# Performance work log

Measured on AMD Instinct MI355X. Metric: run time of the kernel, lower is better.

Reference implementation:

```python
import jax, jax.numpy as jnp
import numpy as np

D_MODEL = 512
NHEAD = 8
HEAD_DIM = D_MODEL // NHEAD
NS = 1  # num_special_tokens


def setup_inputs() -> dict:
    key = jax.random.key(0)
    ks = jax.random.split(key, 12)
    B, N = 8, 1024
    x = jax.random.normal(ks[0], (B, N, D_MODEL), dtype=jnp.float32)
    coords = jax.random.normal(ks[1], (B, N, 3), dtype=jnp.float32) * 5.0
    key_padding_mask = jnp.zeros((B, N), dtype=bool)
    s = 1.0 / np.sqrt(D_MODEL)
    qkv_w = jax.random.normal(ks[2], (3 * D_MODEL, D_MODEL), dtype=jnp.float32) * s
    out_w = jax.random.normal(ks[3], (D_MODEL, D_MODEL), dtype=jnp.float32) * s
    out_b = jnp.zeros((D_MODEL,), dtype=jnp.float32)
    bias_alpha = jnp.ones((1,), dtype=jnp.float32) * 0.5  # nonzero so bias path matters
    w1 = jax.random.normal(ks[4], (NHEAD * 4, 4), dtype=jnp.float32) * 0.5
    b1 = jnp.zeros((NHEAD * 4,), dtype=jnp.float32)
    w2 = jax.random.normal(ks[5], (NHEAD, NHEAD * 4), dtype=jnp.float32) * 0.2
    b2 = jnp.zeros((NHEAD,), dtype=jnp.float32)
    coord_scales = jnp.array([12.0, 12.0, 5.0], dtype=jnp.float32)
    return dict(x=x, coords=coords, key_padding_mask=key_padding_mask,
                qkv_w=qkv_w, out_w=out_w, out_b=out_b, bias_alpha=bias_alpha,
                w1=w1, b1=b1, w2=w2, b2=b2, coord_scales=coord_scales)


def reference(x, coords, key_padding_mask, qkv_w, out_w, out_b, bias_alpha,
              w1, b1, w2, b2, coord_scales):
    B, N, _ = x.shape
    scale = HEAD_DIM ** (-0.5)
    qkv = x @ qkv_w.T  # [B,N,3D]
    q, k, v = jnp.split(qkv, 3, axis=-1)
    def heads(t):
        return t.reshape(B, N, NHEAD, HEAD_DIM).transpose(0, 2, 1, 3)  # [B,H,N,dh]
    q, k, v = heads(q), heads(k), heads(v)

    c = coords / coord_scales  # [B,N,3]
    dpos = c[:, :, None, :] - c[:, None, :, :]  # [B,N,N,3]
    dist = jnp.linalg.norm(dpos, axis=-1, keepdims=True)  # [B,N,N,1]
    feat = jnp.concatenate([dpos, dist], axis=-1)  # [B,N,N,4]
    h = jax.nn.gelu(feat @ w1.T + b1, approximate=False)  # [B,N,N,4H]
    bias = (h @ w2.T + b2).transpose(0, 3, 1, 2)  # [B,H,N,N]
    # zero out bias rows/cols for special tokens
    bias = bias.at[:, :, :NS, :].set(0.0)
    bias = bias.at[:, :, :, :NS].set(0.0)

    dots = jnp.einsum('bhid,bhjd->bhij', q, k) * scale
    logits = dots + bias_alpha * bias
    logits = jnp.where(key_padding_mask[:, None, None, :], -1e30, logits)
    attn = jax.nn.softmax(logits, axis=-1)
    out = jnp.einsum('bhij,bhjd->bhid', attn, v)
    out = out.transpose(0, 2, 1, 3).reshape(B, N, D_MODEL)
    return out @ out_w.T + out_b
```

## Files before the change

### kernel.cpp

```cpp
#include <hip/hip_runtime.h>
#include <math.h>

#define D_MODEL 512
#define NHEAD   8
#define HEAD_DIM 64
#define BB      8
#define NN      1024
#define NS      1
#define TI      16
#define TJ      32
#define NT      (NN / TJ)
#define FIX_M   10.0f
#define GSTRIDE 40

typedef __attribute__((ext_vector_type(8))) short short8;
typedef __attribute__((ext_vector_type(4))) float floatx4;

__device__ __forceinline__ float gelu_fast(float x) {
    const float s = x * 0.70710678118654752f;
    const float u = fabsf(s);
    const float t = __builtin_amdgcn_rcpf(fmaf(0.3275911f, u, 1.0f));
    float p = fmaf(1.061405429f, t, -1.453152027f);
    p = fmaf(p, t, 1.421413741f);
    p = fmaf(p, t, -0.284496736f);
    p = fmaf(p, t, 0.254829592f);
    p = p * t;
    const float e = __expf(-u * u);
    float erf_u = fmaf(-p, e, 1.0f);
    erf_u = copysignf(erf_u, s);
    return 0.5f * x * (1.0f + erf_u);
}

__device__ __forceinline__ unsigned short f2bf(float f) {
    unsigned u = __float_as_uint(f);
    u = (u + 0x7fffu + ((u >> 16) & 1u)) >> 16;
    return (unsigned short)u;
}

__device__ __forceinline__ uint2 pack4bf(float a, float b, float c, float d) {
    uint2 p;
    p.x = (unsigned)f2bf(a) | ((unsigned)f2bf(b) << 16);
    p.y = (unsigned)f2bf(c) | ((unsigned)f2bf(d) << 16);
    return p;
}

__global__ __launch_bounds__(256)
void gemm_qkv_mfma(const float* __restrict__ A, const float* __restrict__ Bm,
                   unsigned short* __restrict__ Qb, unsigned short* __restrict__ Kb,
                   unsigned short* __restrict__ Vt) {
    __shared__ __align__(16) unsigned short As[128 * GSTRIDE];
    __shared__ __align__(16) unsigned short Bs[128 * GSTRIDE];
    const int tid = threadIdx.x;
    const int bm = blockIdx.y * 128;
    const int bn = blockIdx.x * 128;
    const int wv = tid >> 6, lane = tid & 63, quad = lane >> 4, ln = lane & 15;
    const int wm = (wv >> 1) * 64, wn = (wv & 1) * 64;

    floatx4 acc[4][4];
    #pragma unroll
    for (int i = 0; i < 4; ++i)
        #pragma unroll
        for (int j = 0; j < 4; ++j) acc[i][j] = (floatx4){0.f, 0.f, 0.f, 0.f};

    for (int k0 = 0; k0 < 512; k0 += 32) {
        __syncthreads();
        #pragma unroll
        for (int t = 0; t < 4; ++t) {
            const int c = tid + t * 256;
            const int row = c >> 3, kc = (c & 7) * 4;
            float4 v = *(const float4*)(A + (size_t)(bm + row) * 512 + k0 + kc);
            *(uint2*)&As[row * GSTRIDE + kc] = pack4bf(v.x, v.y, v.z, v.w);
            float4 w = *(const float4*)(Bm + (size_t)(bn + row) * 512 + k0 + kc);
            *(uint2*)&Bs[row * GSTRIDE + kc] = pack4bf(w.x, w.y, w.z, w.w);
        }
        __syncthreads();
        short8 af[4], bf[4];
        #pragma unroll
        for (int mb = 0; mb < 4; ++mb)
            af[mb] = *(const short8*)&As[(wm + mb * 16 + ln) * GSTRIDE + quad * 8];
        #pragma unroll
        for (int nb = 0; nb < 4; ++nb)
            bf[nb] = *(const short8*)&Bs[(wn + nb * 16 + ln) * GSTRIDE + quad * 8];
        #pragma unroll
        for (int mb = 0; mb < 4; ++mb)
            #pragma unroll
            for (int nb = 0; nb < 4; ++nb)
                acc[mb][nb] = __builtin_amdgcn_mfma_f32_16x16x32_bf16(af[mb], bf[nb], acc[mb][nb], 0, 0, 0);
    }

    #pragma unroll
    for (int nb = 0; nb < 4; ++nb) {
        const int n = bn + wn + nb * 16 + ln;
        #pragma unroll
        for (int mb = 0; mb < 4; ++mb) {
            const int m = bm + wm + mb * 16 + quad * 4;
            if (n < 512) {
                #pragma unroll
                for (int r = 0; r < 4; ++r)
                    Qb[(size_t)(m + r) * 512 + n] = f2bf(acc[mb][nb][r] * 0.125f);
            } else if (n < 1024) {
                #pragma unroll
                for (int r = 0; r < 4; ++r)
                    Kb[(size_t)(m + r) * 512 + (n - 512)] = f2bf(acc[mb][nb][r]);
            } else {
                const int bb = m >> 10, tok = m & 1023;
                *(uint2*)(Vt + ((size_t)bb * 512 + (n - 1024)) * NN + tok) =
                    pack4bf(acc[mb][nb][0], acc[mb][nb][1], acc[mb][nb][2], acc[mb][nb][3]);
            }
        }
    }
}

__global__ __launch_bounds__(256)
void gemm_out_mfma(const unsigned short* __restrict__ Ab, const float* __restrict__ Bm,
                   const float* __restrict__ bias, float* __restrict__ C) {
    __shared__ __align__(16) unsigned short As[128 * GSTRIDE];
    __shared__ __align__(16) unsigned short Bs[128 * GSTRIDE];
    const int tid = threadIdx.x;
    const int bm = blockIdx.y * 128;
    const int bn = blockIdx.x * 128;
    const int wv = tid >> 6, lane = tid & 63, quad = lane >> 4, ln = lane & 15;
    const int wm = (wv >> 1) * 64, wn = (wv & 1) * 64;

    floatx4 acc[4][4];
    #pragma unroll
    for (int i = 0; i < 4; ++i)
        #pragma unroll
        for (int j = 0; j < 4; ++j) acc[i][j] = (floatx4){0.f, 0.f, 0.f, 0.f};

    for (int k0 = 0; k0 < 512; k0 += 32) {
        __syncthreads();
        #pragma unroll
        for (int t = 0; t < 4; ++t) {
            const int c = tid + t * 256;
            const int row = c >> 3, kc = (c & 7) * 4;
            *(uint2*)&As[row * GSTRIDE + kc] =
                *(const uint2*)(Ab + (size_t)(bm + row) * 512 + k0 + kc);
            float4 w = *(const float4*)(Bm + (size_t)(bn + row) * 512 + k0 + kc);
            *(uint2*)&Bs[row * GSTRIDE + kc] = pack4bf(w.x, w.y, w.z, w.w);
        }
        __syncthreads();
        short8 af[4], bf[4];
        #pragma unroll
        for (int mb = 0; mb < 4; ++mb)
            af[mb] = *(const short8*)&As[(wm + mb * 16 + ln) * GSTRIDE + quad * 8];
        #pragma unroll
        for (int nb = 0; nb < 4; ++nb)
            bf[nb] = *(const short8*)&Bs[(wn + nb * 16 + ln) * GSTRIDE + quad * 8];
        #pragma unroll
        for (int mb = 0; mb < 4; ++mb)
            #pragma unroll
            for (int nb = 0; nb < 4; ++nb)
                acc[mb][nb] = __builtin_amdgcn_mfma_f32_16x16x32_bf16(af[mb], bf[nb], acc[mb][nb], 0, 0, 0);
    }

    #pragma unroll
    for (int nb = 0; nb < 4; ++nb) {
        const int n = bn + wn + nb * 16 + ln;
        const float bv = bias[n];
        #pragma unroll
        for (int mb = 0; mb < 4; ++mb) {
            const int m = bm + wm + mb * 16 + quad * 4;
            #pragma unroll
            for (int r = 0; r < 4; ++r)
                C[(size_t)(m + r) * 512 + n] = acc[mb][nb][r] + bv;
        }
    }
}

#define BIAS_IDX(i, j, h) ((i) * 291 + (j) * 9 + (h))
__global__ __launch_bounds__(256, 2)
void attn_kernel(const unsigned short* __restrict__ Qb,
                 const unsigned short* __restrict__ Kb,
                 const unsigned short* __restrict__ Vt,
                 const float* __restrict__ coords,
                 const unsigned char* __restrict__ mask,
                 const float* __restrict__ w1, const float* __restrict__ b1,
                 const float* __restrict__ w2, const float* __restrict__ b2,
                 const float* __restrict__ coord_scales,
                 const float* __restrict__ alpha_p,
                 unsigned short* __restrict__ attn_out) {
    const int b   = blockIdx.y;
    const int i0  = blockIdx.x * TI;
    const int tid = threadIdx.x;
    const int wv  = tid >> 6;
    const int lane = tid & 63;
    const int quad = lane >> 4;
    const int ln   = lane & 15;
    const int h0   = wv * 2;

    __shared__ float bias_s[2][TI * 291 + 9];
    __shared__ __align__(16) unsigned short ps[NHEAD][TI][40];
    __shared__ float ci_s[TI][3];

    const float alpha = alpha_p[0];
    const float isx = 1.0f / coord_scales[0];
    const float isy = 1.0f / coord_scales[1];
    const float isz = 1.0f / coord_scales[2];

    if (tid < TI * 3)
        ci_s[tid / 3][tid % 3] =
            coords[((size_t)b * NN + i0 + tid / 3) * 3 + tid % 3] / coord_scales[tid % 3];

    float4 w1r[8]; float b1r[8];
    #pragma unroll
    for (int jj = 0; jj < 8; ++jj) {
        w1r[jj] = *(const float4*)(w1 + (quad * 8 + jj) * 4);
        b1r[jj] = b1[quad * 8 + jj];
    }
    short8 b2f;
    #pragma unroll
    for (int jj = 0; jj < 8; ++jj) {
        const float v = (ln < 8) ? alpha * w2[ln * 32 + quad * 8 + jj] : 0.0f;
        b2f[jj] = (short)f2bf(v);
    }
    const float ab2 = (ln < 8) ? alpha * b2[ln] : 0.0f;

    short8 qf[2][2];
    #pragma unroll
    for (int hh = 0; hh < 2; ++hh)
        #pragma unroll
        for (int kd = 0; kd < 2; ++kd)
            qf[hh][kd] = *(const short8*)(Qb + ((size_t)b * NN + i0 + ln) * 512
                                          + (h0 + hh) * 64 + kd * 32 + quad * 8);

    floatx4 oacc[2][4];
    #pragma unroll
    for (int hh = 0; hh < 2; ++hh)
        #pragma unroll
        for (int nd = 0; nd < 4; ++nd)
            oacc[hh][nd] = (floatx4){0.f, 0.f, 0.f, 0.f};
    float l_part[2][4];
    #pragma unroll
    for (int hh = 0; hh < 2; ++hh)
        #pragma unroll
        for (int r = 0; r < 4; ++r) l_part[hh][r] = 0.f;

    const unsigned char* maskp = mask + (size_t)b * NN;
    float cjx[2], cjy[2], cjz[2];

    #define LOAD_CJ(tt_) do { const int tt = (tt_);                               \
        if (tt < NT) {                                                            \
            const float* cp0 = coords + ((size_t)b * NN + tt * TJ + ln) * 3;      \
            cjx[0] = cp0[0] * isx; cjy[0] = cp0[1] * isy; cjz[0] = cp0[2] * isz;  \
            cjx[1] = cp0[48] * isx; cjy[1] = cp0[49] * isy; cjz[1] = cp0[50] * isz; \
        } } while (0)

    #define MLP_TILE(tt_) do { const int tt = (tt_);                              \
        if (tt < NT) {                                                            \
            float* bout = bias_s[tt & 1];                                         \
            const int j0m = tt * TJ;                                              \
            _Pragma("unroll")                                                     \
            for (int g = 0; g < 4; ++g) {                                         \
                const int i = wv * 4 + g;                                         \
                const float cix = ci_s[i][0], ciy = ci_s[i][1], ciz = ci_s[i][2]; \
                const bool irow0 = (i0 + i < NS);                                 \
                _Pragma("unroll")                                                 \
                for (int jh = 0; jh < 2; ++jh) {                                  \
                    const float dx = cix - cjx[jh];                               \
                    const float dy = ciy - cjy[jh];                               \
                    const float dz = ciz - cjz[jh];                               \
                    const float dist = sqrtf(dx * dx + dy * dy + dz * dz);        \
                    short8 hf;                                                    \
                    _Pragma("unroll")                                             \
                    for (int jj = 0; jj < 8; ++jj) {                              \
                        const float4 wa = w1r[jj];                                \
                        float hu = fmaf(wa.x, dx, fmaf(wa.y, dy,                  \
                                   fmaf(wa.z, dz, fmaf(wa.w, dist, b1r[jj]))));   \
                        hu = gelu_fast(hu);                                       \
                        hf[jj] = (short)f2bf(hu);                                 \
                    }                                                             \
                    floatx4 D = __builtin_amdgcn_mfma_f32_16x16x32_bf16(          \
                        hf, b2f, (floatx4){0.f, 0.f, 0.f, 0.f}, 0, 0, 0);         \
                    if (ln < 8) {                                                 \
                        _Pragma("unroll")                                         \
                        for (int r = 0; r < 4; ++r) {                             \
                            const int jw = jh * 16 + quad * 4 + r;                \
                            const float val = (irow0 || (j0m + jw < NS))          \
                                              ? 0.0f : (D[r] + ab2);              \
                            bout[BIAS_IDX(i, jw, ln)] = val;                      \
                        }                                                         \
                    }                                                             \
                }                                                                 \
            }                                                                     \
        } } while (0)

    __syncthreads();
    LOAD_CJ(0);
    MLP_TILE(0);
    __syncthreads();

    for (int jt = 0; jt < NT; ++jt) {
        const int j0 = jt * TJ;
        const int pb = jt & 1;

        short8 kf[2][4], vf[2][4];
        #pragma unroll
        for (int hh = 0; hh < 2; ++hh) {
            const unsigned short* kbase = Kb + ((size_t)b * NN + j0) * 512 + (h0 + hh) * 64;
            kf[hh][0] = *(const short8*)(kbase + (size_t)ln * 512 + quad * 8);
            kf[hh][1] = *(const short8*)(kbase + (size_t)ln * 512 + 32 + quad * 8);
            kf[hh][2] = *(const short8*)(kbase + (size_t)(16 + ln) * 512 + quad * 8);
            kf[hh][3] = *(const short8*)(kbase + (size_t)(16 + ln) * 512 + 32 + quad * 8);
            const unsigned short* vbase = Vt + ((size_t)b * 512 + (h0 + hh) * 64) * NN + j0 + quad * 8;
            #pragma unroll
            for (int nd = 0; nd < 4; ++nd)
                vf[hh][nd] = *(const short8*)(vbase + (size_t)(nd * 16 + ln) * NN);
        }
        const unsigned char mm0 = maskp[j0 + ln];
        const unsigned char mm1 = maskp[j0 + 16 + ln];

        LOAD_CJ(jt + 1);
        MLP_TILE(jt + 1);

        #pragma unroll
        for (int hh = 0; hh < 2; ++hh) {
            const int h = h0 + hh;
            floatx4 s0 = (floatx4){0.f, 0.f, 0.f, 0.f};
            floatx4 s1 = (floatx4){0.f, 0.f, 0.f, 0.f};
            s0 = __builtin_amdgcn_mfma_f32_16x16x32_bf16(qf[hh][0], kf[hh][0], s0, 0, 0, 0);
            s0 = __builtin_amdgcn_mfma_f32_16x16x32_bf16(qf[hh][1], kf[hh][1], s0, 0, 0, 0);
            s1 = __builtin_amdgcn_mfma_f32_16x16x32_bf16(qf[hh][0], kf[hh][2], s1, 0, 0, 0);
            s1 = __builtin_amdgcn_mfma_f32_16x16x32_bf16(qf[hh][1], kf[hh][3], s1, 0, 0, 0);
            #pragma unroll
            for (int r = 0; r < 4; ++r) {
                const int row = quad * 4 + r;
                float v0 = s0[r] + bias_s[pb][BIAS_IDX(row, ln, h)];
                float v1 = s1[r] + bias_s[pb][BIAS_IDX(row, 16 + ln, h)];
                v0 = mm0 ? -1e30f : v0;
                v1 = mm1 ? -1e30f : v1;
                const float e0 = __expf(v0 - FIX_M);
                const float e1 = __expf(v1 - FIX_M);
                l_part[hh][r] += e0 + e1;
                ps[h][row][ln]      = f2bf(e0);
                ps[h][row][16 + ln] = f2bf(e1);
            }
        }

        #pragma unroll
        for (int hh = 0; hh < 2; ++hh) {
            const int h = h0 + hh;
            short8 pa = *(const short8*)&ps[h][ln][quad * 8];
            #pragma unroll
            for (int nd = 0; nd < 4; ++nd)
                oacc[hh][nd] = __builtin_amdgcn_mfma_f32_16x16x32_bf16(pa, vf[hh][nd], oacc[hh][nd], 0, 0, 0);
        }

        __syncthreads();
    }

    #pragma unroll
    for (int hh = 0; hh < 2; ++hh) {
        float rl[4];
        #pragma unroll
        for (int r = 0; r < 4; ++r) {
            float l = l_part[hh][r];
            l += __shfl_xor(l, 1, 64);
            l += __shfl_xor(l, 2, 64);
            l += __shfl_xor(l, 4, 64);
            l += __shfl_xor(l, 8, 64);
            rl[r] = 1.0f / l;
        }
        #pragma unroll
        for (int nd = 0; nd < 4; ++nd)
            #pragma unroll
            for (int r = 0; r < 4; ++r)
                attn_out[((size_t)b * NN + i0 + quad * 4 + r) * 512
                         + (h0 + hh) * 64 + nd * 16 + ln] = f2bf(oacc[hh][nd][r] * rl[r]);
    }
    #undef LOAD_CJ
    #undef MLP_TILE
}

extern "C" void kernel_launch(void* const* d_in, const int* in_sizes, int n_in,
                              void* d_out, int out_size, void* d_ws, size_t ws_size,
                              hipStream_t stream) {
    const float* x        = (const float*)d_in[0];
    const float* coords   = (const float*)d_in[1];
    const unsigned char* kpm = (const unsigned char*)d_in[2];
    const float* qkv_w    = (const float*)d_in[3];
    const float* out_w    = (const float*)d_in[4];
    const float* out_b    = (const float*)d_in[5];
    const float* alpha    = (const float*)d_in[6];
    const float* w1       = (const float*)d_in[7];
    const float* b1       = (const float*)d_in[8];
    const float* w2       = (const float*)d_in[9];
    const float* b2       = (const float*)d_in[10];
    const float* cscales  = (const float*)d_in[11];
    float* out = (float*)d_out;

    const int M = BB * NN;
    unsigned short* Qb = (unsigned short*)d_ws;
    unsigned short* Kb = Qb + (size_t)M * D_MODEL;
    unsigned short* Vt = Kb + (size_t)M * D_MODEL;
    unsigned short* Ao = Vt + (size_t)M * D_MODEL;

    {
        dim3 grid(3 * D_MODEL / 128, M / 128);
        gemm_qkv_mfma<<<grid, 256, 0, stream>>>(x, qkv_w, Qb, Kb, Vt);
    }
    {
        dim3 grid(NN / TI, BB);
        attn_kernel<<<grid, 256, 0, stream>>>(Qb, Kb, Vt, coords, kpm, w1, b1, w2, b2,
                                              cscales, alpha, Ao);
    }
    {
        dim3 grid(D_MODEL / 128, M / 128);
        gemm_out_mfma<<<grid, 256, 0, stream>>>(Ao, out_w, out_b, out);
    }
}
```

Baseline: 422.3 us.

## Split attention key range across two blocks and merge partials in output GEMM

The attention grid gains a z dimension that splits the key tiles into two halves. Each half writes unnormalized fp32 partial outputs and row sums, which works because softmax uses a fixed max. The output projection GEMM now loads both partials, adds them, normalizes by the summed denominators and converts to bf16 while staging its A tile. Launch bounds for the attention kernel rise to three blocks per CU to raise occupancy. The cost is extra fp32 workspace traffic and a possible register-pressure penalty.

```diff
diff --git a/kernel.cpp b/kernel.cpp
--- a/kernel.cpp
+++ b/kernel.cpp
@@ -112,7 +112,9 @@
 }
 
 __global__ __launch_bounds__(256)
-void gemm_out_mfma(const unsigned short* __restrict__ Ab, const float* __restrict__ Bm,
+void gemm_out_mfma(const float* __restrict__ O0, const float* __restrict__ O1,
+                   const float* __restrict__ l0, const float* __restrict__ l1,
+                   const float* __restrict__ Bm,
                    const float* __restrict__ bias, float* __restrict__ C) {
     __shared__ __align__(16) unsigned short As[128 * GSTRIDE];
     __shared__ __align__(16) unsigned short Bs[128 * GSTRIDE];
@@ -134,9 +136,17 @@
         for (int t = 0; t < 4; ++t) {
             const int c = tid + t * 256;
             const int row = c >> 3, kc = (c & 7) * 4;
+            const int tok = bm + row;
+            const int kk = k0 + kc;
+            const int hd = kk >> 6;
+            float4 a0 = *(const float4*)(O0 + (size_t)tok * 512 + kk);
+            float4 a1 = *(const float4*)(O1 + (size_t)tok * 512 + kk);
+            const float ls = l0[tok * 8 + hd] + l1[tok * 8 + hd];
+            const float ri = __builtin_amdgcn_rcpf(ls);
             *(uint2*)&As[row * GSTRIDE + kc] =
-                *(const uint2*)(Ab + (size_t)(bm + row) * 512 + k0 + kc);
-            float4 w = *(const float4*)(Bm + (size_t)(bn + row) * 512 + k0 + kc);
+                pack4bf((a0.x + a1.x) * ri, (a0.y + a1.y) * ri,
+                        (a0.z + a1.z) * ri, (a0.w + a1.w) * ri);
+            float4 w = *(const float4*)(Bm + (size_t)(bn + row) * 512 + kk);
             *(uint2*)&Bs[row * GSTRIDE + kc] = pack4bf(w.x, w.y, w.z, w.w);
         }
         __syncthreads();
@@ -169,7 +179,7 @@
 }
 
 #define BIAS_IDX(i, j, h) ((i) * 291 + (j) * 9 + (h))
-__global__ __launch_bounds__(256, 2)
+__global__ __launch_bounds__(256, 3)
 void attn_kernel(const unsigned short* __restrict__ Qb,
                  const unsigned short* __restrict__ Kb,
                  const unsigned short* __restrict__ Vt,
@@ -179,7 +189,7 @@
                  const float* __restrict__ w2, const float* __restrict__ b2,
                  const float* __restrict__ coord_scales,
                  const float* __restrict__ alpha_p,
-                 unsigned short* __restrict__ attn_out) {
+                 float* __restrict__ Opart, float* __restrict__ lpart) {
     const int b   = blockIdx.y;
     const int i0  = blockIdx.x * TI;
     const int tid = threadIdx.x;
@@ -188,6 +198,11 @@
     const int quad = lane >> 4;
     const int ln   = lane & 15;
     const int h0   = wv * 2;
+    const int t0t  = blockIdx.z * (NT / 2);
+    const int tlim = t0t + NT / 2;
+
+    float* __restrict__ Op = Opart + (size_t)blockIdx.z * BB * NN * 512;
+    float* __restrict__ lp = lpart + (size_t)blockIdx.z * BB * NN * 8;
 
     __shared__ float bias_s[2][TI * 291 + 9];
     __shared__ __align__(16) unsigned short ps[NHEAD][TI][40];
@@ -240,14 +255,14 @@
     float cjx[2], cjy[2], cjz[2];
 
     #define LOAD_CJ(tt_) do { const int tt = (tt_);                               \
-        if (tt < NT) {                                                            \
+        if (tt < tlim) {                                                          \
             const float* cp0 = coords + ((size_t)b * NN + tt * TJ + ln) * 3;      \
             cjx[0] = cp0[0] * isx; cjy[0] = cp0[1] * isy; cjz[0] = cp0[2] * isz;  \
             cjx[1] = cp0[48] * isx; cjy[1] = cp0[49] * isy; cjz[1] = cp0[50] * isz; \
         } } while (0)
 
     #define MLP_TILE(tt_) do { const int tt = (tt_);                              \
-        if (tt < NT) {                                                            \
+        if (tt < tlim) {                                                          \
             float* bout = bias_s[tt & 1];                                         \
             const int j0m = tt * TJ;                                              \
             _Pragma("unroll")                                                     \
@@ -286,11 +301,11 @@
         } } while (0)
 
     __syncthreads();
-    LOAD_CJ(0);
-    MLP_TILE(0);
+    LOAD_CJ(t0t);
+    MLP_TILE(t0t);
     __syncthreads();
 
-    for (int jt = 0; jt < NT; ++jt) {
+    for (int jt = t0t; jt < tlim; ++jt) {
         const int j0 = jt * TJ;
         const int pb = jt & 1;
 
@@ -351,7 +366,6 @@
 
     #pragma unroll
     for (int hh = 0; hh < 2; ++hh) {
-        float rl[4];
         #pragma unroll
         for (int r = 0; r < 4; ++r) {
             float l = l_part[hh][r];
@@ -359,14 +373,15 @@
             l += __shfl_xor(l, 2, 64);
             l += __shfl_xor(l, 4, 64);
             l += __shfl_xor(l, 8, 64);
-            rl[r] = 1.0f / l;
+            if (ln == 0)
+                lp[((size_t)b * NN + i0 + quad * 4 + r) * 8 + (h0 + hh)] = l;
         }
         #pragma unroll
         for (int nd = 0; nd < 4; ++nd)
             #pragma unroll
             for (int r = 0; r < 4; ++r)
-                attn_out[((size_t)b * NN + i0 + quad * 4 + r) * 512
-                         + (h0 + hh) * 64 + nd * 16 + ln] = f2bf(oacc[hh][nd][r] * rl[r]);
+                Op[((size_t)b * NN + i0 + quad * 4 + r) * 512
+                   + (h0 + hh) * 64 + nd * 16 + ln] = oacc[hh][nd][r];
     }
     #undef LOAD_CJ
     #undef MLP_TILE
@@ -393,19 +408,22 @@
     unsigned short* Qb = (unsigned short*)d_ws;
     unsigned short* Kb = Qb + (size_t)M * D_MODEL;
     unsigned short* Vt = Kb + (size_t)M * D_MODEL;
-    unsigned short* Ao = Vt + (size_t)M * D_MODEL;
+    float* O0 = (float*)(Vt + (size_t)M * D_MODEL);
+    float* O1 = O0 + (size_t)M * D_MODEL;
+    float* l0 = O1 + (size_t)M * D_MODEL;
+    float* l1 = l0 + (size_t)M * NHEAD;
 
     {
         dim3 grid(3 * D_MODEL / 128, M / 128);
         gemm_qkv_mfma<<<grid, 256, 0, stream>>>(x, qkv_w, Qb, Kb, Vt);
     }
     {
-        dim3 grid(NN / TI, BB);
+        dim3 grid(NN / TI, BB, 2);
         attn_kernel<<<grid, 256, 0, stream>>>(Qb, Kb, Vt, coords, kpm, w1, b1, w2, b2,
-                                              cscales, alpha, Ao);
+                                              cscales, alpha, O0, l0);
     }
     {
         dim3 grid(D_MODEL / 128, M / 128);
-        gemm_out_mfma<<<grid, 256, 0, stream>>>(Ao, out_w, out_b, out);
-    }
-}
+        gemm_out_mfma<<<grid, 256, 0, stream>>>(O0, O1, l0, l1, out_w, out_b, out);
+    }
+}
```

Result: slower. 615.6 us (+45.8%).

## Use one wave per head in attention kernel with 512-thread blocks

Applied to the files above, without the earlier changes.

The attention kernel now launches 512 threads (8 waves) per block, with each wave owning a single head instead of two. The coordinate-MLP bias work per wave is halved to two rows per tile. This cuts per-thread register state (Q fragments, accumulators, K/V fragments) and raises wave-level parallelism per block. The cost is a larger block, more threads meeting at each __syncthreads, and an occupancy set by the new launch bounds of (512,4) instead of (256,2).

```diff
diff --git a/kernel.cpp b/kernel.cpp
--- a/kernel.cpp
+++ b/kernel.cpp
@@ -169,7 +169,7 @@
 }
 
 #define BIAS_IDX(i, j, h) ((i) * 291 + (j) * 9 + (h))
-__global__ __launch_bounds__(256, 2)
+__global__ __launch_bounds__(512, 4)
 void attn_kernel(const unsigned short* __restrict__ Qb,
                  const unsigned short* __restrict__ Kb,
                  const unsigned short* __restrict__ Vt,
@@ -183,11 +183,10 @@
     const int b   = blockIdx.y;
     const int i0  = blockIdx.x * TI;
     const int tid = threadIdx.x;
-    const int wv  = tid >> 6;
+    const int h   = tid >> 6;
     const int lane = tid & 63;
     const int quad = lane >> 4;
     const int ln   = lane & 15;
-    const int h0   = wv * 2;
 
     __shared__ float bias_s[2][TI * 291 + 9];
     __shared__ __align__(16) unsigned short ps[NHEAD][TI][40];
@@ -216,25 +215,16 @@
     }
     const float ab2 = (ln < 8) ? alpha * b2[ln] : 0.0f;
 
-    short8 qf[2][2];
-    #pragma unroll
-    for (int hh = 0; hh < 2; ++hh)
-        #pragma unroll
-        for (int kd = 0; kd < 2; ++kd)
-            qf[hh][kd] = *(const short8*)(Qb + ((size_t)b * NN + i0 + ln) * 512
-                                          + (h0 + hh) * 64 + kd * 32 + quad * 8);
-
-    floatx4 oacc[2][4];
-    #pragma unroll
-    for (int hh = 0; hh < 2; ++hh)
-        #pragma unroll
-        for (int nd = 0; nd < 4; ++nd)
-            oacc[hh][nd] = (floatx4){0.f, 0.f, 0.f, 0.f};
-    float l_part[2][4];
-    #pragma unroll
-    for (int hh = 0; hh < 2; ++hh)
-        #pragma unroll
-        for (int r = 0; r < 4; ++r) l_part[hh][r] = 0.f;
+    short8 qf[2];
+    #pragma unroll
+    for (int kd = 0; kd < 2; ++kd)
+        qf[kd] = *(const short8*)(Qb + ((size_t)b * NN + i0 + ln) * 512
+                                  + h * 64 + kd * 32 + quad * 8);
+
+    floatx4 oacc[4];
+    #pragma unroll
+    for (int nd = 0; nd < 4; ++nd) oacc[nd] = (floatx4){0.f, 0.f, 0.f, 0.f};
+    float l_part[4] = {0.f, 0.f, 0.f, 0.f};
 
     const unsigned char* maskp = mask + (size_t)b * NN;
     float cjx[2], cjy[2], cjz[2];
@@ -251,8 +241,8 @@
             float* bout = bias_s[tt & 1];                                         \
             const int j0m = tt * TJ;                                              \
             _Pragma("unroll")                                                     \
-            for (int g = 0; g < 4; ++g) {                                         \
-                const int i = wv * 4 + g;                                         \
+            for (int g = 0; g < 2; ++g) {                                         \
+                const int i = h * 2 + g;                                          \
                 const float cix = ci_s[i][0], ciy = ci_s[i][1], ciz = ci_s[i][2]; \
                 const bool irow0 = (i0 + i < NS);                                 \
                 _Pragma("unroll")                                                 \
@@ -294,18 +284,17 @@
         const int j0 = jt * TJ;
         const int pb = jt & 1;
 
-        short8 kf[2][4], vf[2][4];
-        #pragma unroll
-        for (int hh = 0; hh < 2; ++hh) {
-            const unsigned short* kbase = Kb + ((size_t)b * NN + j0) * 512 + (h0 + hh) * 64;
-            kf[hh][0] = *(const short8*)(kbase + (size_t)ln * 512 + quad * 8);
-            kf[hh][1] = *(const short8*)(kbase + (size_t)ln * 512 + 32 + quad * 8);
-            kf[hh][2] = *(const short8*)(kbase + (size_t)(16 + ln) * 512 + quad * 8);
-            kf[hh][3] = *(const short8*)(kbase + (size_t)(16 + ln) * 512 + 32 + quad * 8);
-            const unsigned short* vbase = Vt + ((size_t)b * 512 + (h0 + hh) * 64) * NN + j0 + quad * 8;
+        short8 kf[4], vf[4];
+        {
+            const unsigned short* kbase = Kb + ((size_t)b * NN + j0) * 512 + h * 64;
+            kf[0] = *(const short8*)(kbase + (size_t)ln * 512 + quad * 8);
+            kf[1] = *(const short8*)(kbase + (size_t)ln * 512 + 32 + quad * 8);
+            kf[2] = *(const short8*)(kbase + (size_t)(16 + ln) * 512 + quad * 8);
+            kf[3] = *(const short8*)(kbase + (size_t)(16 + ln) * 512 + 32 + quad * 8);
+            const unsigned short* vbase = Vt + ((size_t)b * 512 + h * 64) * NN + j0 + quad * 8;
             #pragma unroll
             for (int nd = 0; nd < 4; ++nd)
-                vf[hh][nd] = *(const short8*)(vbase + (size_t)(nd * 16 + ln) * NN);
+                vf[nd] = *(const short8*)(vbase + (size_t)(nd * 16 + ln) * NN);
         }
         const unsigned char mm0 = maskp[j0 + ln];
         const unsigned char mm1 = maskp[j0 + 16 + ln];
@@ -313,15 +302,13 @@
         LOAD_CJ(jt + 1);
         MLP_TILE(jt + 1);
 
-        #pragma unroll
-        for (int hh = 0; hh < 2; ++hh) {
-            const int h = h0 + hh;
+        {
             floatx4 s0 = (floatx4){0.f, 0.f, 0.f, 0.f};
             floatx4 s1 = (floatx4){0.f, 0.f, 0.f, 0.f};
-            s0 = __builtin_amdgcn_mfma_f32_16x16x32_bf16(qf[hh][0], kf[hh][0], s0, 0, 0, 0);
-            s0 = __builtin_amdgcn_mfma_f32_16x16x32_bf16(qf[hh][1], kf[hh][1], s0, 0, 0, 0);
-            s1 = __builtin_amdgcn_mfma_f32_16x16x32_bf16(qf[hh][0], kf[hh][2], s1, 0, 0, 0);
-            s1 = __builtin_amdgcn_mfma_f32_16x16x32_bf16(qf[hh][1], kf[hh][3], s1, 0, 0, 0);
+            s0 = __builtin_amdgcn_mfma_f32_16x16x32_bf16(qf[0], kf[0], s0, 0, 0, 0);
+            s0 = __builtin_amdgcn_mfma_f32_16x16x32_bf16(qf[1], kf[1], s0, 0, 0, 0);
+            s1 = __builtin_amdgcn_mfma_f32_16x16x32_bf16(qf[0], kf[2], s1, 0, 0, 0);
+            s1 = __builtin_amdgcn_mfma_f32_16x16x32_bf16(qf[1], kf[3], s1, 0, 0, 0);
             #pragma unroll
             for (int r = 0; r < 4; ++r) {
                 const int row = quad * 4 + r;
@@ -331,30 +318,27 @@
                 v1 = mm1 ? -1e30f : v1;
                 const float e0 = __expf(v0 - FIX_M);
                 const float e1 = __expf(v1 - FIX_M);
-                l_part[hh][r] += e0 + e1;
+                l_part[r] += e0 + e1;
                 ps[h][row][ln]      = f2bf(e0);
                 ps[h][row][16 + ln] = f2bf(e1);
             }
         }
 
-        #pragma unroll
-        for (int hh = 0; hh < 2; ++hh) {
-            const int h = h0 + hh;
+        {
             short8 pa = *(const short8*)&ps[h][ln][quad * 8];
             #pragma unroll
             for (int nd = 0; nd < 4; ++nd)
-                oacc[hh][nd] = __builtin_amdgcn_mfma_f32_16x16x32_bf16(pa, vf[hh][nd], oacc[hh][nd], 0, 0, 0);
-        }
-
-        __syncthreads();
-    }
-
-    #pragma unroll
-    for (int hh = 0; hh < 2; ++hh) {
+                oacc[nd] = __builtin_amdgcn_mfma_f32_16x16x32_bf16(pa, vf[nd], oacc[nd], 0, 0, 0);
+        }
+
+        __syncthreads();
+    }
+
+    {
         float rl[4];
         #pragma unroll
         for (int r = 0; r < 4; ++r) {
-            float l = l_part[hh][r];
+            float l = l_part[r];
             l += __shfl_xor(l, 1, 64);
             l += __shfl_xor(l, 2, 64);
             l += __shfl_xor(l, 4, 64);
@@ -366,7 +350,7 @@
             #pragma unroll
             for (int r = 0; r < 4; ++r)
                 attn_out[((size_t)b * NN + i0 + quad * 4 + r) * 512
-                         + (h0 + hh) * 64 + nd * 16 + ln] = f2bf(oacc[hh][nd][r] * rl[r]);
+                         + h * 64 + nd * 16 + ln] = f2bf(oacc[nd][r] * rl[r]);
     }
     #undef LOAD_CJ
     #undef MLP_TILE
@@ -401,7 +385,7 @@
     }
     {
         dim3 grid(NN / TI, BB);
-        attn_kernel<<<grid, 256, 0, stream>>>(Qb, Kb, Vt, coords, kpm, w1, b1, w2, b2,
+        attn_kernel<<<grid, 512, 0, stream>>>(Qb, Kb, Vt, coords, kpm, w1, b1, w2, b2,
                                               cscales, alpha, Ao);
     }
     {
```

New measurement: 568.4 us. +34.6%, slower.

## Split attention key range across two wave groups with 512-thread blocks

Applied to the files above, without the earlier changes.

The attention kernel now launches 512 threads per block. Two groups of four waves each handle half of the key tiles, with separate bias and probability buffers per half. The partial output accumulators and row sums are merged through shared memory at the end. This doubles the waves available to hide the serial per-tile MLP bias, softmax and MFMA chain, at the cost of a final reduction, an extra barrier per tile, loss of the previous double-buffered overlap between MLP and compute, and higher register pressure under launch_bounds(512,2).

```diff
diff --git a/kernel.cpp b/kernel.cpp
--- a/kernel.cpp
+++ b/kernel.cpp
@@ -10,6 +10,7 @@
 #define TI      16
 #define TJ      32
 #define NT      (NN / TJ)
+#define NTH     (NT / 2)
 #define FIX_M   10.0f
 #define GSTRIDE 40
 
@@ -169,7 +170,7 @@
 }
 
 #define BIAS_IDX(i, j, h) ((i) * 291 + (j) * 9 + (h))
-__global__ __launch_bounds__(256, 2)
+__global__ __launch_bounds__(512, 2)
 void attn_kernel(const unsigned short* __restrict__ Qb,
                  const unsigned short* __restrict__ Kb,
                  const unsigned short* __restrict__ Vt,
@@ -180,17 +181,20 @@
                  const float* __restrict__ coord_scales,
                  const float* __restrict__ alpha_p,
                  unsigned short* __restrict__ attn_out) {
-    const int b   = blockIdx.y;
-    const int i0  = blockIdx.x * TI;
-    const int tid = threadIdx.x;
-    const int wv  = tid >> 6;
+    const int b    = blockIdx.y;
+    const int i0   = blockIdx.x * TI;
+    const int tid  = threadIdx.x;
+    const int wv   = tid >> 6;
+    const int half = wv >> 2;
+    const int wq   = wv & 3;
     const int lane = tid & 63;
     const int quad = lane >> 4;
     const int ln   = lane & 15;
-    const int h0   = wv * 2;
+    const int h0   = wq * 2;
+    const int tbase = half * NTH;
 
     __shared__ float bias_s[2][TI * 291 + 9];
-    __shared__ __align__(16) unsigned short ps[NHEAD][TI][40];
+    __shared__ __align__(16) unsigned short ps[2][NHEAD][TI][40];
     __shared__ float ci_s[TI][3];
 
     const float alpha = alpha_p[0];
@@ -238,21 +242,42 @@
 
     const unsigned char* maskp = mask + (size_t)b * NN;
     float cjx[2], cjy[2], cjz[2];
-
-    #define LOAD_CJ(tt_) do { const int tt = (tt_);                               \
-        if (tt < NT) {                                                            \
-            const float* cp0 = coords + ((size_t)b * NN + tt * TJ + ln) * 3;      \
+    short8 kf[2][4], vf[2][4];
+    int mm0 = 0, mm1 = 0;
+
+    #define LOAD_CJ(t_) do { const int t2 = (t_);                                 \
+        if (t2 < NTH) {                                                           \
+            const float* cp0 = coords + ((size_t)b * NN + (tbase + t2) * TJ + ln) * 3; \
             cjx[0] = cp0[0] * isx; cjy[0] = cp0[1] * isy; cjz[0] = cp0[2] * isz;  \
             cjx[1] = cp0[48] * isx; cjy[1] = cp0[49] * isy; cjz[1] = cp0[50] * isz; \
         } } while (0)
 
-    #define MLP_TILE(tt_) do { const int tt = (tt_);                              \
-        if (tt < NT) {                                                            \
-            float* bout = bias_s[tt & 1];                                         \
-            const int j0m = tt * TJ;                                              \
+    #define LOADS(t_) do { const int t2 = (t_);                                   \
+        if (t2 < NTH) {                                                           \
+            const int j0l = (tbase + t2) * TJ;                                    \
+            _Pragma("unroll")                                                     \
+            for (int hh = 0; hh < 2; ++hh) {                                      \
+                const unsigned short* kbase = Kb + ((size_t)b * NN + j0l) * 512 + (h0 + hh) * 64; \
+                kf[hh][0] = *(const short8*)(kbase + (size_t)ln * 512 + quad * 8);        \
+                kf[hh][1] = *(const short8*)(kbase + (size_t)ln * 512 + 32 + quad * 8);   \
+                kf[hh][2] = *(const short8*)(kbase + (size_t)(16 + ln) * 512 + quad * 8); \
+                kf[hh][3] = *(const short8*)(kbase + (size_t)(16 + ln) * 512 + 32 + quad * 8); \
+                const unsigned short* vbase = Vt + ((size_t)b * 512 + (h0 + hh) * 64) * NN + j0l + quad * 8; \
+                _Pragma("unroll")                                                 \
+                for (int nd = 0; nd < 4; ++nd)                                    \
+                    vf[hh][nd] = *(const short8*)(vbase + (size_t)(nd * 16 + ln) * NN); \
+            }                                                                     \
+            mm0 = maskp[j0l + ln];                                                \
+            mm1 = maskp[j0l + 16 + ln];                                           \
+        } } while (0)
+
+    #define MLP_TILE(t_) do { const int t2 = (t_);                                \
+        if (t2 < NTH) {                                                           \
+            float* bout = bias_s[half];                                           \
+            const int j0m = (tbase + t2) * TJ;                                    \
             _Pragma("unroll")                                                     \
             for (int g = 0; g < 4; ++g) {                                         \
-                const int i = wv * 4 + g;                                         \
+                const int i = wq * 4 + g;                                         \
                 const float cix = ci_s[i][0], ciy = ci_s[i][1], ciz = ci_s[i][2]; \
                 const bool irow0 = (i0 + i < NS);                                 \
                 _Pragma("unroll")                                                 \
@@ -288,31 +313,10 @@
     __syncthreads();
     LOAD_CJ(0);
     MLP_TILE(0);
+    LOADS(0);
     __syncthreads();
 
-    for (int jt = 0; jt < NT; ++jt) {
-        const int j0 = jt * TJ;
-        const int pb = jt & 1;
-
-        short8 kf[2][4], vf[2][4];
-        #pragma unroll
-        for (int hh = 0; hh < 2; ++hh) {
-            const unsigned short* kbase = Kb + ((size_t)b * NN + j0) * 512 + (h0 + hh) * 64;
-            kf[hh][0] = *(const short8*)(kbase + (size_t)ln * 512 + quad * 8);
-            kf[hh][1] = *(const short8*)(kbase + (size_t)ln * 512 + 32 + quad * 8);
-            kf[hh][2] = *(const short8*)(kbase + (size_t)(16 + ln) * 512 + quad * 8);
-            kf[hh][3] = *(const short8*)(kbase + (size_t)(16 + ln) * 512 + 32 + quad * 8);
-            const unsigned short* vbase = Vt + ((size_t)b * 512 + (h0 + hh) * 64) * NN + j0 + quad * 8;
-            #pragma unroll
-            for (int nd = 0; nd < 4; ++nd)
-                vf[hh][nd] = *(const short8*)(vbase + (size_t)(nd * 16 + ln) * NN);
-        }
-        const unsigned char mm0 = maskp[j0 + ln];
-        const unsigned char mm1 = maskp[j0 + 16 + ln];
-
-        LOAD_CJ(jt + 1);
-        MLP_TILE(jt + 1);
-
+    for (int t = 0; t < NTH; ++t) {
         #pragma unroll
         for (int hh = 0; hh < 2; ++hh) {
             const int h = h0 + hh;
@@ -325,33 +329,37 @@
             #pragma unroll
             for (int r = 0; r < 4; ++r) {
                 const int row = quad * 4 + r;
-                float v0 = s0[r] + bias_s[pb][BIAS_IDX(row, ln, h)];
-                float v1 = s1[r] + bias_s[pb][BIAS_IDX(row, 16 + ln, h)];
+                float v0 = s0[r] + bias_s[half][BIAS_IDX(row, ln, h)];
+                float v1 = s1[r] + bias_s[half][BIAS_IDX(row, 16 + ln, h)];
                 v0 = mm0 ? -1e30f : v0;
                 v1 = mm1 ? -1e30f : v1;
                 const float e0 = __expf(v0 - FIX_M);
                 const float e1 = __expf(v1 - FIX_M);
                 l_part[hh][r] += e0 + e1;
-                ps[h][row][ln]      = f2bf(e0);
-                ps[h][row][16 + ln] = f2bf(e1);
+                ps[half][h][row][ln]      = f2bf(e0);
+                ps[half][h][row][16 + ln] = f2bf(e1);
             }
         }
 
         #pragma unroll
         for (int hh = 0; hh < 2; ++hh) {
             const int h = h0 + hh;
-            short8 pa = *(const short8*)&ps[h][ln][quad * 8];
+            short8 pa = *(const short8*)&ps[half][h][ln][quad * 8];
             #pragma unroll
             for (int nd = 0; nd < 4; ++nd)
                 oacc[hh][nd] = __builtin_amdgcn_mfma_f32_16x16x32_bf16(pa, vf[hh][nd], oacc[hh][nd], 0, 0, 0);
         }
 
         __syncthreads();
-    }
-
-    #pragma unroll
-    for (int hh = 0; hh < 2; ++hh) {
-        float rl[4];
+        LOADS(t + 1);
+        LOAD_CJ(t + 1);
+        MLP_TILE(t + 1);
+        __syncthreads();
+    }
+
+    float l_red[2][4];
+    #pragma unroll
+    for (int hh = 0; hh < 2; ++hh)
         #pragma unroll
         for (int r = 0; r < 4; ++r) {
             float l = l_part[hh][r];
@@ -359,16 +367,46 @@
             l += __shfl_xor(l, 2, 64);
             l += __shfl_xor(l, 4, 64);
             l += __shfl_xor(l, 8, 64);
-            rl[r] = 1.0f / l;
-        }
-        #pragma unroll
-        for (int nd = 0; nd < 4; ++nd)
+            l_red[hh][r] = l;
+        }
+
+    float* Osc = &bias_s[0][0];
+    float* lsc = Osc + 8320;
+    if (half == 1) {
+        #pragma unroll
+        for (int hh = 0; hh < 2; ++hh) {
+            #pragma unroll
+            for (int nd = 0; nd < 4; ++nd)
+                #pragma unroll
+                for (int r = 0; r < 4; ++r)
+                    Osc[((h0 + hh) * 16 + quad * 4 + r) * 65 + nd * 16 + ln] = oacc[hh][nd][r];
+            if (ln == 0)
+                #pragma unroll
+                for (int r = 0; r < 4; ++r)
+                    lsc[(h0 + hh) * 16 + quad * 4 + r] = l_red[hh][r];
+        }
+    }
+    __syncthreads();
+    if (half == 0) {
+        #pragma unroll
+        for (int hh = 0; hh < 2; ++hh) {
+            float rl[4];
             #pragma unroll
             for (int r = 0; r < 4; ++r)
-                attn_out[((size_t)b * NN + i0 + quad * 4 + r) * 512
-                         + (h0 + hh) * 64 + nd * 16 + ln] = f2bf(oacc[hh][nd][r] * rl[r]);
+                rl[r] = 1.0f / (l_red[hh][r] + lsc[(h0 + hh) * 16 + quad * 4 + r]);
+            #pragma unroll
+            for (int nd = 0; nd < 4; ++nd)
+                #pragma unroll
+                for (int r = 0; r < 4; ++r) {
+                    const float o1 = Osc[((h0 + hh) * 16 + quad * 4 + r) * 65 + nd * 16 + ln];
+                    attn_out[((size_t)b * NN + i0 + quad * 4 + r) * 512
+                             + (h0 + hh) * 64 + nd * 16 + ln] =
+                        f2bf((oacc[hh][nd][r] + o1) * rl[r]);
+                }
+        }
     }
     #undef LOAD_CJ
+    #undef LOADS
     #undef MLP_TILE
 }
 
@@ -401,7 +439,7 @@
     }
     {
         dim3 grid(NN / TI, BB);
-        attn_kernel<<<grid, 256, 0, stream>>>(Qb, Kb, Vt, coords, kpm, w1, b1, w2, b2,
+        attn_kernel<<<grid, 512, 0, stream>>>(Qb, Kb, Vt, coords, kpm, w1, b1, w2, b2,
                                               cscales, alpha, Ao);
     }
     {
```

New measurement: 466.5 us. +10.5%, slower.
